# Kernel optimization log

Hardware: AMD Instinct MI355X
Metric: run time of the kernel (lower is better)

The kernel has to match this reference:

```python
import jax, jax.numpy as jnp
import numpy as np


def setup_inputs() -> dict:
    key = jax.random.key(0)
    k1, k2, k3, k4 = jax.random.split(key, 4)
    N, E, F_IN, H, C = 100000, 1600000, 128, 64, 64
    x = jax.random.normal(k1, (N, F_IN), dtype=jnp.float32)
    edge_index = jax.random.randint(k2, (2, E), 0, N, dtype=jnp.int64)
    W1 = jax.random.normal(k3, (F_IN, H), dtype=jnp.float32) / np.sqrt(F_IN)
    b1 = jnp.zeros((H,), dtype=jnp.float32)
    W2 = jax.random.normal(k4, (H, C), dtype=jnp.float32) / np.sqrt(H)
    b2 = jnp.zeros((C,), dtype=jnp.float32)
    return {"x": x, "edge_index": edge_index, "W1": W1, "b1": b1, "W2": W2, "b2": b2}


def reference(x, edge_index, W1, b1, W2, b2):
    N = x.shape[0]
    # add self-loops (PyG GCNConv default)
    loop = jnp.arange(N, dtype=edge_index.dtype)
    src = jnp.concatenate([edge_index[0], loop])
    dst = jnp.concatenate([edge_index[1], loop])
    # symmetric normalization: deg^{-1/2}[src] * deg^{-1/2}[dst], deg over dst
    deg = jax.ops.segment_sum(jnp.ones_like(dst, dtype=x.dtype), dst, num_segments=N)
    dis = jnp.where(deg > 0, jax.lax.rsqrt(deg), 0.0)
    norm = dis[src] * dis[dst]  # [E+N]

    def gcn_conv(h, W, b):
        h = h @ W                                   # [N, out]
        msg = h[src] * norm[:, None]                # [E+N, out] gather
        agg = jax.ops.segment_sum(msg, dst, num_segments=N)  # scatter-add
        return agg + b

    h = jax.nn.relu(gcn_conv(x, W1, b1))
    # dropout inactive in eval mode
    out = gcn_conv(h, W2, b2)
    return jax.nn.log_softmax(out, axis=1)
```

## Files before the change

kernel.cpp:

```cpp
#include <hip/hip_runtime.h>
#include <cstdint>
#include <cstddef>

#define PASSA_EDGES 8192
#define PASSB_CAP   12288


__device__ __forceinline__ unsigned short f2bf(float f) {
    unsigned int u = __float_as_uint(f);
    u += 0x7FFFu + ((u >> 16) & 1u);
    return (unsigned short)(u >> 16);
}

__device__ __forceinline__ void bf8_fma(uint4 u, float w, float* acc) {
    acc[0] += __uint_as_float(u.x << 16) * w;
    acc[1] += __uint_as_float(u.x & 0xFFFF0000u) * w;
    acc[2] += __uint_as_float(u.y << 16) * w;
    acc[3] += __uint_as_float(u.y & 0xFFFF0000u) * w;
    acc[4] += __uint_as_float(u.z << 16) * w;
    acc[5] += __uint_as_float(u.z & 0xFFFF0000u) * w;
    acc[6] += __uint_as_float(u.w << 16) * w;
    acc[7] += __uint_as_float(u.w & 0xFFFF0000u) * w;
}
__device__ __forceinline__ void bf8_unpack(uint4 u, float* v) {
    v[0] = __uint_as_float(u.x << 16);
    v[1] = __uint_as_float(u.x & 0xFFFF0000u);
    v[2] = __uint_as_float(u.y << 16);
    v[3] = __uint_as_float(u.y & 0xFFFF0000u);
    v[4] = __uint_as_float(u.z << 16);
    v[5] = __uint_as_float(u.z & 0xFFFF0000u);
    v[6] = __uint_as_float(u.w << 16);
    v[7] = __uint_as_float(u.w & 0xFFFF0000u);
}


__global__ void bcur_init(int* __restrict__ bcur, int NBUCK, int CAP) {
    int b = threadIdx.x;
    if (b < NBUCK) bcur[b] = b * CAP;
}


__global__ __launch_bounds__(256) void passA(const int* __restrict__ src,
                                             const int* __restrict__ dst,
                                             int* __restrict__ bcur,
                                             int2* __restrict__ bbuf, int E,
                                             int CAP, int shift) {
    __shared__ int2 bins[PASSA_EDGES];
    __shared__ int  cnt[256], off[256], cur[256], gbase[256];
    const int t  = threadIdx.x;
    const int e0 = blockIdx.x * PASSA_EDGES;
    const int n  = min(PASSA_EDGES, E - e0);

    cnt[t] = 0;
    __syncthreads();
    for (int i = t; i < n; i += 256) atomicAdd(&cnt[dst[e0 + i] >> shift], 1);
    __syncthreads();

    int v = cnt[t];
    off[t] = v;
    __syncthreads();
    for (int o = 1; o < 256; o <<= 1) {
        int u = (t >= o) ? off[t - o] : 0;
        __syncthreads();
        off[t] += u;
        __syncthreads();
    }
    int excl = off[t] - v;
    off[t]   = excl;
    cur[t]   = excl;
    __syncthreads();

    for (int i = t; i < n; i += 256) {
        int d = dst[e0 + i];
        int s = src[e0 + i];
        int p = atomicAdd(&cur[d >> shift], 1);
        bins[p] = make_int2(s, d);
    }
    if (cnt[t] > 0) gbase[t] = atomicAdd(&bcur[t], cnt[t]);
    __syncthreads();

    const int w = t >> 6, lane = t & 63;
    for (int b = w; b < 256; b += 4) {
        int c = cnt[b];
        if (c == 0) continue;
        int lo  = off[b], go = gbase[b];
        int lim = (b + 1) * CAP;
        if (go + c > lim) c = max(0, lim - go);
        for (int i = lane; i < c; i += 64) bbuf[go + i] = bins[lo + i];
    }
}


__global__ __launch_bounds__(256) void hist_dis(const int2* __restrict__ bbuf,
                                                const int* __restrict__ bcur,
                                                int* __restrict__ hist,
                                                float* __restrict__ dis,
                                                int N, int CAP, int shift) {
    __shared__ int cnt[1024];
    const int b     = blockIdx.x;
    const int node0 = b << shift;
    const int nn    = min(1 << shift, N - node0);
    for (int j = threadIdx.x; j < nn; j += 256) cnt[j] = 0;
    __syncthreads();
    const int start = b * CAP, end = bcur[b];
    for (int e = start + threadIdx.x; e < end; e += 256)
        atomicAdd(&cnt[bbuf[e].y - node0], 1);
    __syncthreads();
    for (int j = threadIdx.x; j < nn; j += 256) {
        int c = cnt[j];
        hist[node0 + j] = c;
        dis[node0 + j]  = rsqrtf((float)(c + 1));
    }
}


__global__ __launch_bounds__(256) void scan_partial(const int* __restrict__ hist,
                                                    int* __restrict__ partials, int N) {
    __shared__ int red[256];
    const int t    = threadIdx.x;
    const int base = blockIdx.x * 1024 + t * 4;
    int s = 0;
    if (base + 3 < N) {
        int4 v = *(const int4*)&hist[base];
        s = v.x + v.y + v.z + v.w;
    } else {
        for (int i = 0; i < 4; i++)
            if (base + i < N) s += hist[base + i];
    }
    red[t] = s;
    __syncthreads();
    for (int off = 128; off; off >>= 1) {
        if (t < off) red[t] += red[t + off];
        __syncthreads();
    }
    if (t == 0) partials[blockIdx.x] = red[0];
}

__global__ __launch_bounds__(256) void scan_offsets(int* __restrict__ partials, int NB) {
    __shared__ int tmp[256];
    const int t = threadIdx.x;
    int v = (t < NB) ? partials[t] : 0;
    tmp[t] = v;
    __syncthreads();
    for (int off = 1; off < 256; off <<= 1) {
        int u = (t >= off) ? tmp[t - off] : 0;
        __syncthreads();
        tmp[t] += u;
        __syncthreads();
    }
    if (t < NB) partials[t] = tmp[t] - v;
}

__global__ __launch_bounds__(256) void scan_apply(const int* __restrict__ hist,
                                                  const int* __restrict__ partials,
                                                  int* __restrict__ ptr, int N) {
    __shared__ int tsum[256];
    const int t    = threadIdx.x;
    const int base = blockIdx.x * 1024 + t * 4;
    int v[4];
    int s = 0;
    for (int i = 0; i < 4; i++) {
        v[i] = (base + i < N) ? hist[base + i] : 0;
        s += v[i];
    }
    tsum[t] = s;
    __syncthreads();
    for (int off = 1; off < 256; off <<= 1) {
        int u = (t >= off) ? tsum[t - off] : 0;
        __syncthreads();
        tsum[t] += u;
        __syncthreads();
    }
    int run = partials[blockIdx.x] + tsum[t] - s;
    for (int i = 0; i < 4; i++) {
        if (base + i < N) {
            ptr[base + i] = run;
            run += v[i];
        }
    }
    if (base <= N - 1 && N - 1 < base + 4) ptr[N] = run;
}


__global__ __launch_bounds__(256) void passB(const int2* __restrict__ bbuf,
                                             const int* __restrict__ bcur,
                                             const int* __restrict__ ptr,
                                             int2* __restrict__ csrw,
                                             const float* __restrict__ dis,
                                             int N, int CAP, int shift) {
    __shared__ int lcnt[1024];
    __shared__ int lcsr[PASSB_CAP];
    const int b     = blockIdx.x;
    const int node0 = b << shift;
    const int nn    = min(1 << shift, N - node0);
    const int cbase = ptr[node0];
    const int csize = ptr[node0 + nn] - cbase;

    for (int j = threadIdx.x; j < nn; j += 256) lcnt[j] = ptr[node0 + j] - cbase;
    __syncthreads();

    const int start = b * CAP, end = bcur[b];
    if (csize <= PASSB_CAP) {
        for (int e = start + threadIdx.x; e < end; e += 256) {
            int2 pr = bbuf[e];
            int  p  = atomicAdd(&lcnt[pr.y - node0], 1);
            lcsr[p] = pr.x;
        }
        __syncthreads();
        for (int i = threadIdx.x; i < csize; i += 256) {
            int s = lcsr[i];
            csrw[cbase + i] = make_int2(s, __float_as_int(dis[s]));
        }
    } else {
        for (int e = start + threadIdx.x; e < end; e += 256) {
            int2 pr = bbuf[e];
            int  p  = atomicAdd(&lcnt[pr.y - node0], 1);
            csrw[cbase + p] = make_int2(pr.x, __float_as_int(dis[pr.x]));
        }
    }
}


template <int K>
__global__ __launch_bounds__(256) void gemm64_bf16(const float* __restrict__ X,
                                                   const float* __restrict__ W,
                                                   unsigned short* __restrict__ Yb, int N) {
    constexpr int LDX = K + 4;
    __shared__ float xs[64 * LDX];
    __shared__ float ws[K * 64];
    const int tid  = threadIdx.x;
    const int row0 = blockIdx.x * 64;

    const float4* W4 = (const float4*)W;
    for (int i = tid; i < K * 16; i += 256) ((float4*)ws)[i] = W4[i];

    const float4* X4  = (const float4*)(X + (size_t)row0 * K);
    const int     nf4 = (row0 < N ? min(64, N - row0) : 0) * (K / 4);
    for (int i = tid; i < 16 * K; i += 256) {
        float4 v = make_float4(0.f, 0.f, 0.f, 0.f);
        if (i < nf4) v = X4[i];
        int r  = i / (K / 4);
        int kk = (i % (K / 4)) * 4;
        *(float4*)&xs[r * LDX + kk] = v;
    }
    __syncthreads();

    const int cg = tid & 15;
    const int rg = tid >> 4;

    float acc[4][4] = {};
#pragma unroll 2
    for (int k = 0; k < K; k += 4) {
        float4 xf[4], wf[4];
#pragma unroll
        for (int i = 0; i < 4; i++) xf[i] = *(const float4*)&xs[(rg * 4 + i) * LDX + k];
#pragma unroll
        for (int j = 0; j < 4; j++) wf[j] = *(const float4*)&ws[(k + j) * 64 + cg * 4];
#pragma unroll
        for (int i = 0; i < 4; i++) {
            float4 xv = xf[i];
            acc[i][0] += xv.x * wf[0].x + xv.y * wf[1].x + xv.z * wf[2].x + xv.w * wf[3].x;
            acc[i][1] += xv.x * wf[0].y + xv.y * wf[1].y + xv.z * wf[2].y + xv.w * wf[3].y;
            acc[i][2] += xv.x * wf[0].z + xv.y * wf[1].z + xv.z * wf[2].z + xv.w * wf[3].z;
            acc[i][3] += xv.x * wf[0].w + xv.y * wf[1].w + xv.z * wf[2].w + xv.w * wf[3].w;
        }
    }

#pragma unroll
    for (int i = 0; i < 4; i++) {
        int r = row0 + rg * 4 + i;
        if (r < N) {
            ushort4 o;
            o.x = f2bf(acc[i][0]); o.y = f2bf(acc[i][1]);
            o.z = f2bf(acc[i][2]); o.w = f2bf(acc[i][3]);
            *(ushort4*)&Yb[(size_t)r * 64 + cg * 4] = o;
        }
    }
}


__device__ __forceinline__ void gather8_oct(const unsigned short* __restrict__ B,
                                            const int2* __restrict__ csrw,
                                            int s0, int s1, int iters,
                                            int lane, int co, float* acc) {
    int  e  = s0 + co;
    int2 pv = make_int2(0, 0);
    if (e < s1) pv = csrw[e];
    for (int it = 0; it < iters; ++it) {
        const int en = e + 8;
        int2      pn = make_int2(0, 0);
        if (it + 1 < iters && en < s1) pn = csrw[en];
        const int   sv = pv.x;
        const float wv = __int_as_float(pv.y);
        int   s_[8];
        float w_[8];
#pragma unroll
        for (int i = 0; i < 8; i++) {
            const int srcl = (lane & 56) | i;
            s_[i] = __shfl(sv, srcl);
            w_[i] = __shfl(wv, srcl);
        }
        uint4 u_[8];
#pragma unroll
        for (int i = 0; i < 8; i++)
            u_[i] = *(const uint4*)&B[(size_t)s_[i] * 64 + co * 8];
#pragma unroll
        for (int i = 0; i < 8; i++) bf8_fma(u_[i], w_[i], acc);
        pv = pn;
        e  = en;
    }
}


__global__ __launch_bounds__(256) void agg_l1(const unsigned short* __restrict__ B,
                                              const int2* __restrict__ csrw,
                                              const int* __restrict__ ptr,
                                              const float* __restrict__ dis,
                                              const float* __restrict__ b1,
                                              const float* __restrict__ W2,
                                              unsigned short* __restrict__ hw, int N) {
    __shared__ float w2s[64 * 64];
    for (int i = threadIdx.x; i < 1024; i += 256)
        ((float4*)w2s)[i] = ((const float4*)W2)[i];
    __syncthreads();

    const int wid  = threadIdx.x >> 6;
    const int lane = threadIdx.x & 63;
    const int eg   = lane >> 3;
    const int co   = lane & 7;
    const int eg2  = lane >> 4;
    const int cq   = lane & 15;

    const int  rbase = blockIdx.x * 32 + wid * 8;
    const int  row   = rbase + eg;
    const bool hr    = (row < N);

    const int   s0 = hr ? ptr[row] : 0;
    const int   s1 = hr ? ptr[row + 1] : 0;
    const float di = hr ? dis[row] : 0.f;
    const int   iters = (s1 - s0 + 7) >> 3;

    float acc[8] = {};
    gather8_oct(B, csrw, s0, s1, iters, lane, co, acc);

    float h[8] = {};
    if (hr) {
        uint4 us = *(const uint4*)&B[(size_t)row * 64 + co * 8];
        float bs[8];
        bf8_unpack(us, bs);
        float bb[8];
        *(float4*)&bb[0] = *(const float4*)&b1[co * 8];
        *(float4*)&bb[4] = *(const float4*)&b1[co * 8 + 4];
#pragma unroll
        for (int i = 0; i < 8; i++)
            h[i] = fmaxf((acc[i] + bs[i] * di) * di + bb[i], 0.f);
    }

    for (int r = 0; r < 8; ++r) {
        const int rr = rbase + r;
        if (rr >= N) break;
        float o[4] = {0.f, 0.f, 0.f, 0.f};
#pragma unroll
        for (int j = 0; j < 16; j++) {
            const int    k    = eg2 * 16 + j;
            const int    srcl = r * 8 + eg2 * 2 + (j >> 3);
            const float  hk   = __shfl(h[j & 7], srcl);
            const float4 wr   = *(const float4*)&w2s[k * 64 + cq * 4];
            o[0] += hk * wr.x;
            o[1] += hk * wr.y;
            o[2] += hk * wr.z;
            o[3] += hk * wr.w;
        }
#pragma unroll
        for (int off = 16; off <= 32; off <<= 1)
#pragma unroll
            for (int i = 0; i < 4; i++) o[i] += __shfl_xor(o[i], off);

        if (eg2 == 0) {
            ushort4 ob;
            ob.x = f2bf(o[0]); ob.y = f2bf(o[1]);
            ob.z = f2bf(o[2]); ob.w = f2bf(o[3]);
            *(ushort4*)&hw[(size_t)rr * 64 + cq * 4] = ob;
        }
    }
}


__global__ __launch_bounds__(256) void agg_l2(const unsigned short* __restrict__ B,
                                              const int2* __restrict__ csrw,
                                              const int* __restrict__ ptr,
                                              const float* __restrict__ dis,
                                              const float* __restrict__ b2,
                                              float* __restrict__ out, int N) {
    const int wid  = threadIdx.x >> 6;
    const int lane = threadIdx.x & 63;
    const int eg   = lane >> 3;
    const int co   = lane & 7;

    const int  row = blockIdx.x * 32 + wid * 8 + eg;
    const bool hr  = (row < N);

    const int   s0 = hr ? ptr[row] : 0;
    const int   s1 = hr ? ptr[row + 1] : 0;
    const float di = hr ? dis[row] : 0.f;
    const int   iters = (s1 - s0 + 7) >> 3;

    float acc[8] = {};
    gather8_oct(B, csrw, s0, s1, iters, lane, co, acc);

    if (!hr) return;

    uint4 us = *(const uint4*)&B[(size_t)row * 64 + co * 8];
    float bs[8];
    bf8_unpack(us, bs);
    float bb[8];
    *(float4*)&bb[0] = *(const float4*)&b2[co * 8];
    *(float4*)&bb[4] = *(const float4*)&b2[co * 8 + 4];

    float v[8];
#pragma unroll
    for (int i = 0; i < 8; i++) v[i] = (acc[i] + bs[i] * di) * di + bb[i];

    float m = v[0];
#pragma unroll
    for (int i = 1; i < 8; i++) m = fmaxf(m, v[i]);
#pragma unroll
    for (int off = 1; off <= 4; off <<= 1) m = fmaxf(m, __shfl_xor(m, off));
    float s = 0.f;
#pragma unroll
    for (int i = 0; i < 8; i++) s += __expf(v[i] - m);
#pragma unroll
    for (int off = 1; off <= 4; off <<= 1) s += __shfl_xor(s, off);
    float lse = m + __logf(s);

    float4 oa = make_float4(v[0] - lse, v[1] - lse, v[2] - lse, v[3] - lse);
    float4 ob = make_float4(v[4] - lse, v[5] - lse, v[6] - lse, v[7] - lse);
    *(float4*)&out[(size_t)row * 64 + co * 8]     = oa;
    *(float4*)&out[(size_t)row * 64 + co * 8 + 4] = ob;
}


extern "C" void kernel_launch(void* const* d_in, const int* in_sizes, int n_in,
                              void* d_out, int out_size, void* d_ws, size_t ws_size,
                              hipStream_t stream) {
    const float* x   = (const float*)d_in[0];
    const int*   ei  = (const int*)d_in[1];
    const float* W1  = (const float*)d_in[2];
    const float* b1  = (const float*)d_in[3];
    const float* W2  = (const float*)d_in[4];
    const float* b2  = (const float*)d_in[5];
    float*       out = (float*)d_out;

    const int  N   = in_sizes[0] / 128;
    const int  E   = in_sizes[1] / 2;
    const int* src = ei;
    const int* dst = ei + E;
    const int  NB  = (N + 1023) / 1024;

    int shift = 9;
    while (((N - 1) >> shift) >= 256) shift++;
    const int NBUCK = ((N - 1) >> shift) + 1;
    const int CAP   = ((E / NBUCK) * 3 / 2 + 255) & ~255;

    auto align256 = [](size_t v) { return (v + 255) & ~(size_t)255; };
    char*           p        = (char*)d_ws;
    float*          dis      = (float*)p;          p += align256((size_t)N * 4);
    int*            ptr      = (int*)p;            p += align256((size_t)(N + 1) * 4);
    int*            hist     = (int*)p;            p += align256((size_t)N * 4);
    int*            partials = (int*)p;            p += align256((size_t)NB * 4);
    int*            bcur     = (int*)p;            p += align256(256 * 4);
    int2*           csrw     = (int2*)p;           p += align256((size_t)E * 8);
    int2*           bbuf     = (int2*)p;           p += align256((size_t)NBUCK * CAP * 8);
    unsigned short* xwb      = (unsigned short*)p; p += align256((size_t)N * 64 * 2);
    unsigned short* hwb      = (unsigned short*)p; p += align256((size_t)N * 64 * 2);

    bcur_init<<<1, 256, 0, stream>>>(bcur, NBUCK, CAP);
    passA<<<(E + PASSA_EDGES - 1) / PASSA_EDGES, 256, 0, stream>>>(src, dst, bcur, bbuf, E, CAP, shift);
    hist_dis<<<NBUCK, 256, 0, stream>>>(bbuf, bcur, hist, dis, N, CAP, shift);
    scan_partial<<<NB, 256, 0, stream>>>(hist, partials, N);
    scan_offsets<<<1, 256, 0, stream>>>(partials, NB);
    scan_apply<<<NB, 256, 0, stream>>>(hist, partials, ptr, N);
    passB<<<NBUCK, 256, 0, stream>>>(bbuf, bcur, ptr, csrw, dis, N, CAP, shift);

    gemm64_bf16<128><<<(N + 63) / 64, 256, 0, stream>>>(x, W1, xwb, N);
    agg_l1<<<(N + 31) / 32, 256, 0, stream>>>(xwb, csrw, ptr, dis, b1, W2, hwb, N);
    agg_l2<<<(N + 31) / 32, 256, 0, stream>>>(hwb, csrw, ptr, dis, b2, out, N);
}
```

Measured before the change: 289.5 us.

## Pad CSR rows to multiples of eight and split W2 GEMM out of aggregation

Each node's in-degree is rounded up to a multiple of eight and the padding slots are filled with zero-weight entries pointing at node 0. This lets the gather loop read edge pairs as vectorized int4 loads with no shuffles or bounds checks. The fused W2 projection inside agg_l1 is removed. agg_l1 now writes fp32 hidden activations into the output buffer as scratch, and a separate gemm64_bf16<64> pass computes the layer-2 features. In exchange it adds padding traffic (extra gathers of node 0 and a larger CSR), an extra fp32 round trip of the hidden layer through memory, and one more kernel launch.

Result: no change. 285.9 us (-1.2%).

```diff
diff --git a/kernel.cpp b/kernel.cpp
--- a/kernel.cpp
+++ b/kernel.cpp
@@ -108,7 +108,7 @@
     __syncthreads();
     for (int j = threadIdx.x; j < nn; j += 256) {
         int c = cnt[j];
-        hist[node0 + j] = c;
+        hist[node0 + j] = (c + 7) & ~7;
         dis[node0 + j]  = rsqrtf((float)(c + 1));
     }
 }
@@ -201,6 +201,8 @@
 
     const int start = b * CAP, end = bcur[b];
     if (csize <= PASSB_CAP) {
+        for (int i = threadIdx.x; i < csize; i += 256) lcsr[i] = -1;
+        __syncthreads();
         for (int e = start + threadIdx.x; e < end; e += 256) {
             int2 pr = bbuf[e];
             int  p  = atomicAdd(&lcnt[pr.y - node0], 1);
@@ -209,9 +211,12 @@
         __syncthreads();
         for (int i = threadIdx.x; i < csize; i += 256) {
             int s = lcsr[i];
-            csrw[cbase + i] = make_int2(s, __float_as_int(dis[s]));
+            csrw[cbase + i] = (s < 0) ? make_int2(0, 0)
+                                      : make_int2(s, __float_as_int(dis[s]));
         }
     } else {
+        for (int i = threadIdx.x; i < csize; i += 256) csrw[cbase + i] = make_int2(0, 0);
+        __syncthreads();
         for (int e = start + threadIdx.x; e < end; e += 256) {
             int2 pr = bbuf[e];
             int  p  = atomicAdd(&lcnt[pr.y - node0], 1);
@@ -279,35 +284,32 @@
 }
 
 
-__device__ __forceinline__ void gather8_oct(const unsigned short* __restrict__ B,
+__device__ __forceinline__ void gather8_pad(const unsigned short* __restrict__ B,
                                             const int2* __restrict__ csrw,
-                                            int s0, int s1, int iters,
-                                            int lane, int co, float* acc) {
-    int  e  = s0 + co;
-    int2 pv = make_int2(0, 0);
-    if (e < s1) pv = csrw[e];
+                                            int s0, int iters, int co, float* acc) {
+    const int4* cs = (const int4*)(csrw + s0);
+    int4 c0 = make_int4(0, 0, 0, 0), c1 = c0, c2 = c0, c3 = c0;
+    if (iters > 0) { c0 = cs[0]; c1 = cs[1]; c2 = cs[2]; c3 = cs[3]; }
     for (int it = 0; it < iters; ++it) {
-        const int en = e + 8;
-        int2      pn = make_int2(0, 0);
-        if (it + 1 < iters && en < s1) pn = csrw[en];
-        const int   sv = pv.x;
-        const float wv = __int_as_float(pv.y);
-        int   s_[8];
-        float w_[8];
-#pragma unroll
-        for (int i = 0; i < 8; i++) {
-            const int srcl = (lane & 56) | i;
-            s_[i] = __shfl(sv, srcl);
-            w_[i] = __shfl(wv, srcl);
-        }
-        uint4 u_[8];
-#pragma unroll
-        for (int i = 0; i < 8; i++)
-            u_[i] = *(const uint4*)&B[(size_t)s_[i] * 64 + co * 8];
-#pragma unroll
-        for (int i = 0; i < 8; i++) bf8_fma(u_[i], w_[i], acc);
-        pv = pn;
-        e  = en;
+        const int nb = min(it + 1, iters - 1) * 4;
+        int4 n0 = cs[nb], n1 = cs[nb + 1], n2 = cs[nb + 2], n3 = cs[nb + 3];
+        uint4 u0 = *(const uint4*)&B[(size_t)c0.x * 64 + co * 8];
+        uint4 u1 = *(const uint4*)&B[(size_t)c0.z * 64 + co * 8];
+        uint4 u2 = *(const uint4*)&B[(size_t)c1.x * 64 + co * 8];
+        uint4 u3 = *(const uint4*)&B[(size_t)c1.z * 64 + co * 8];
+        uint4 u4 = *(const uint4*)&B[(size_t)c2.x * 64 + co * 8];
+        uint4 u5 = *(const uint4*)&B[(size_t)c2.z * 64 + co * 8];
+        uint4 u6 = *(const uint4*)&B[(size_t)c3.x * 64 + co * 8];
+        uint4 u7 = *(const uint4*)&B[(size_t)c3.z * 64 + co * 8];
+        bf8_fma(u0, __int_as_float(c0.y), acc);
+        bf8_fma(u1, __int_as_float(c0.w), acc);
+        bf8_fma(u2, __int_as_float(c1.y), acc);
+        bf8_fma(u3, __int_as_float(c1.w), acc);
+        bf8_fma(u4, __int_as_float(c2.y), acc);
+        bf8_fma(u5, __int_as_float(c2.w), acc);
+        bf8_fma(u6, __int_as_float(c3.y), acc);
+        bf8_fma(u7, __int_as_float(c3.w), acc);
+        c0 = n0; c1 = n1; c2 = n2; c3 = n3;
     }
 }
 
@@ -317,72 +319,39 @@
                                               const int* __restrict__ ptr,
                                               const float* __restrict__ dis,
                                               const float* __restrict__ b1,
-                                              const float* __restrict__ W2,
-                                              unsigned short* __restrict__ hw, int N) {
-    __shared__ float w2s[64 * 64];
-    for (int i = threadIdx.x; i < 1024; i += 256)
-        ((float4*)w2s)[i] = ((const float4*)W2)[i];
-    __syncthreads();
-
+                                              float* __restrict__ hs, int N) {
     const int wid  = threadIdx.x >> 6;
     const int lane = threadIdx.x & 63;
     const int eg   = lane >> 3;
     const int co   = lane & 7;
-    const int eg2  = lane >> 4;
-    const int cq   = lane & 15;
-
-    const int  rbase = blockIdx.x * 32 + wid * 8;
-    const int  row   = rbase + eg;
-    const bool hr    = (row < N);
+
+    const int  row = blockIdx.x * 32 + wid * 8 + eg;
+    const bool hr  = (row < N);
 
     const int   s0 = hr ? ptr[row] : 0;
     const int   s1 = hr ? ptr[row + 1] : 0;
     const float di = hr ? dis[row] : 0.f;
-    const int   iters = (s1 - s0 + 7) >> 3;
+    const int   iters = (s1 - s0) >> 3;
 
     float acc[8] = {};
-    gather8_oct(B, csrw, s0, s1, iters, lane, co, acc);
-
-    float h[8] = {};
-    if (hr) {
-        uint4 us = *(const uint4*)&B[(size_t)row * 64 + co * 8];
-        float bs[8];
-        bf8_unpack(us, bs);
-        float bb[8];
-        *(float4*)&bb[0] = *(const float4*)&b1[co * 8];
-        *(float4*)&bb[4] = *(const float4*)&b1[co * 8 + 4];
-#pragma unroll
-        for (int i = 0; i < 8; i++)
-            h[i] = fmaxf((acc[i] + bs[i] * di) * di + bb[i], 0.f);
-    }
-
-    for (int r = 0; r < 8; ++r) {
-        const int rr = rbase + r;
-        if (rr >= N) break;
-        float o[4] = {0.f, 0.f, 0.f, 0.f};
-#pragma unroll
-        for (int j = 0; j < 16; j++) {
-            const int    k    = eg2 * 16 + j;
-            const int    srcl = r * 8 + eg2 * 2 + (j >> 3);
-            const float  hk   = __shfl(h[j & 7], srcl);
-            const float4 wr   = *(const float4*)&w2s[k * 64 + cq * 4];
-            o[0] += hk * wr.x;
-            o[1] += hk * wr.y;
-            o[2] += hk * wr.z;
-            o[3] += hk * wr.w;
-        }
-#pragma unroll
-        for (int off = 16; off <= 32; off <<= 1)
-#pragma unroll
-            for (int i = 0; i < 4; i++) o[i] += __shfl_xor(o[i], off);
-
-        if (eg2 == 0) {
-            ushort4 ob;
-            ob.x = f2bf(o[0]); ob.y = f2bf(o[1]);
-            ob.z = f2bf(o[2]); ob.w = f2bf(o[3]);
-            *(ushort4*)&hw[(size_t)rr * 64 + cq * 4] = ob;
-        }
-    }
+    gather8_pad(B, csrw, s0, iters, co, acc);
+
+    if (!hr) return;
+
+    uint4 us = *(const uint4*)&B[(size_t)row * 64 + co * 8];
+    float bs[8];
+    bf8_unpack(us, bs);
+    float bb[8];
+    *(float4*)&bb[0] = *(const float4*)&b1[co * 8];
+    *(float4*)&bb[4] = *(const float4*)&b1[co * 8 + 4];
+
+    float h[8];
+#pragma unroll
+    for (int i = 0; i < 8; i++)
+        h[i] = fmaxf((acc[i] + bs[i] * di) * di + bb[i], 0.f);
+
+    *(float4*)&hs[(size_t)row * 64 + co * 8]     = make_float4(h[0], h[1], h[2], h[3]);
+    *(float4*)&hs[(size_t)row * 64 + co * 8 + 4] = make_float4(h[4], h[5], h[6], h[7]);
 }
 
 
@@ -403,10 +372,10 @@
     const int   s0 = hr ? ptr[row] : 0;
     const int   s1 = hr ? ptr[row + 1] : 0;
     const float di = hr ? dis[row] : 0.f;
-    const int   iters = (s1 - s0 + 7) >> 3;
+    const int   iters = (s1 - s0) >> 3;
 
     float acc[8] = {};
-    gather8_oct(B, csrw, s0, s1, iters, lane, co, acc);
+    gather8_pad(B, csrw, s0, iters, co, acc);
 
     if (!hr) return;
 
@@ -469,10 +438,12 @@
     int*            hist     = (int*)p;            p += align256((size_t)N * 4);
     int*            partials = (int*)p;            p += align256((size_t)NB * 4);
     int*            bcur     = (int*)p;            p += align256(256 * 4);
-    int2*           csrw     = (int2*)p;           p += align256((size_t)E * 8);
+    int2*           csrw     = (int2*)p;           p += align256(((size_t)E + 8 * (size_t)N) * 8);
     int2*           bbuf     = (int2*)p;           p += align256((size_t)NBUCK * CAP * 8);
     unsigned short* xwb      = (unsigned short*)p; p += align256((size_t)N * 64 * 2);
     unsigned short* hwb      = (unsigned short*)p; p += align256((size_t)N * 64 * 2);
+
+    float* hs = out;
 
     bcur_init<<<1, 256, 0, stream>>>(bcur, NBUCK, CAP);
     passA<<<(E + PASSA_EDGES - 1) / PASSA_EDGES, 256, 0, stream>>>(src, dst, bcur, bbuf, E, CAP, shift);
@@ -483,6 +454,7 @@
     passB<<<NBUCK, 256, 0, stream>>>(bbuf, bcur, ptr, csrw, dis, N, CAP, shift);
 
     gemm64_bf16<128><<<(N + 63) / 64, 256, 0, stream>>>(x, W1, xwb, N);
-    agg_l1<<<(N + 31) / 32, 256, 0, stream>>>(xwb, csrw, ptr, dis, b1, W2, hwb, N);
-    agg_l2<<<(N + 31) / 32, 256, 0, stream>>>(hwb, csrw, ptr, dis, b2, out, N);
-}
+    agg_l1<<<(N + 31) / 32, 256, 0, stream>>>(xwb, csrw, ptr, dis, b1, hs, N);
+    gemm64_bf16<64><<<(N + 63) / 64, 256, 0, stream>>>(hs, W2, xwb, N);
+    agg_l2<<<(N + 31) / 32, 256, 0, stream>>>(xwb, csrw, ptr, dis, b2, out, N);
+}
```
